# Kernel optimization log

Hardware: AMD Instinct MI355X
Metric: run time of the kernel (lower is better)

Reference implementation:

```python
import jax, jax.numpy as jnp
import numpy as np

# dims: B=8, T=12, N=512, F_in=64, H=8, F'=out_features//H=8
NEG_SLOPE = 0.01  # torch LeakyReLU default


def setup_inputs() -> dict:
    key = jax.random.key(0)
    ks = jax.random.split(key, 8)
    B, T, N, Fin, H, Fp = 8, 12, 512, 64, 8, 8
    x = jax.random.normal(ks[0], (B, T, N, Fin), dtype=jnp.float32)
    # sparse-ish adjacency with guaranteed self loops (avoids all -inf rows)
    adj = (jax.random.uniform(ks[1], (N, N)) < 0.05).astype(jnp.float32)
    adj = jnp.clip(adj + jnp.eye(N, dtype=jnp.float32), 0.0, 1.0)
    # per-head Linear(in_features, F'): stacked weights [H, Fin, F'] + bias [H, F']
    W = jax.random.normal(ks[2], (H, Fin, Fp), dtype=jnp.float32) * 0.1
    Wb = jax.random.normal(ks[3], (H, Fp), dtype=jnp.float32) * 0.1
    # per-head Linear(2F', 1): split into src-half a1 (multiplies h_j, first F'
    # of the concat) and dst-half a2 (multiplies h_i), plus scalar bias ab
    a1 = jax.random.normal(ks[4], (H, Fp), dtype=jnp.float32) * 0.1
    a2 = jax.random.normal(ks[5], (H, Fp), dtype=jnp.float32) * 0.1
    ab = jax.random.normal(ks[6], (H,), dtype=jnp.float32) * 0.1
    return {"x": x, "adj": adj, "W": W, "Wb": Wb, "a1": a1, "a2": a2, "ab": ab}


def reference(x, adj, W, Wb, a1, a2, ab):
    # h[b,t,h,n,f'] = x @ W_h + b_h
    h = jnp.einsum('btni,hio->bthno', x, W) + Wb[:, None, :]
    # a(cat(h_j, h_i)) = a1.h_j + a2.h_i + ab  (exact decomposition of the
    # original broadcast-concat; avoids the O(N^2 * 2F') a_input tensor)
    s_src = jnp.einsum('bthno,ho->bthn', h, a1)  # contributes along j axis
    s_dst = jnp.einsum('bthno,ho->bthn', h, a2)  # contributes along i axis
    e = jax.nn.leaky_relu(
        s_src[..., None, :] + s_dst[..., :, None] + ab[:, None, None],
        negative_slope=NEG_SLOPE,
    )  # [B,T,H,N,N]
    e = jnp.where(adj == 0, -jnp.inf, e)
    attn = jax.nn.softmax(e, axis=-1)  # (dropout is identity in eval mode)
    h_prime = jnp.einsum('bthij,bthjo->bthio', attn, h)  # [B,T,H,N,F']
    B, T, H, N, Fp = h_prime.shape
    # concat heads along feature dim, matching torch.cat(head_outputs, -1)
    return h_prime.transpose(0, 1, 3, 2, 4).reshape(B, T, N, H * Fp)
```

## Files before the change

### kernel.cpp

```cpp
#include <hip/hip_runtime.h>
#include <math.h>

namespace {

constexpr int kN    = 512;
constexpr int kFin  = 64;
constexpr int kH    = 8;
constexpr int kFp   = 8;
constexpr int kBT   = 96;
constexpr int kNT   = 256;
constexpr int kMaxDeg = 104;
constexpr float kNeg = 0.01f;
constexpr float kL2E = 1.44269504088896340736f;

typedef _Float16 half8t __attribute__((ext_vector_type(8)));
typedef unsigned int uint;

__device__ __forceinline__ float fast_exp2(float v) {
#if __has_builtin(__builtin_amdgcn_exp2f)
  return __builtin_amdgcn_exp2f(v);
#else
  return exp2f(v);
#endif
}

constexpr int kOffBits = 0;
constexpr int kOffPerm = kOffBits + kN * 16;
constexpr int kOffDeg  = kOffPerm + kN;
constexpr int kOffRPos = kOffDeg + kN;
constexpr int kOffIdx  = kOffRPos + kN;

__global__ void pack_adj_kernel(const float* __restrict__ adj,
                                uint* __restrict__ bitsR) {
  const int t = blockIdx.x * blockDim.x + threadIdx.x;
  const unsigned long long m = __ballot(adj[t] != 0.0f);
  const int lane = threadIdx.x & 63;
  if ((lane & 31) == 0) {
    const int i = t >> 9;
    const int w = (t & 511) >> 5;
    bitsR[i * 16 + w] = (uint)(m >> (lane & 32));
  }
}

__global__ __launch_bounds__(512) void sort_assign_kernel(
    const uint* __restrict__ bitsR, uint* __restrict__ permG,
    uint* __restrict__ degG, uint* __restrict__ rowpos) {
  __shared__ int base[128];
  const int i = threadIdx.x;
  int deg = 0;
#pragma unroll
  for (int w = 0; w < 16; ++w) deg += __popc(bitsR[i * 16 + w]);
  const int dc = min(deg, 127);

  if (i < 128) base[i] = 0;
  __syncthreads();
  atomicAdd(&base[dc], 1);
  __syncthreads();
  if (i == 0) {
    int run = 0;
    for (int k = 0; k < 128; ++k) {
      const int c = base[k];
      base[k] = run;
      run += c;
    }
  }
  __syncthreads();
  const int pos = atomicAdd(&base[dc], 1);
  permG[pos] = (uint)i;
  degG[pos] = (uint)deg;
  rowpos[i] = (uint)pos;
}

__global__ __launch_bounds__(64) void csr_fill_kernel(
    const uint* __restrict__ bitsR, const uint* __restrict__ rowpos,
    uint* __restrict__ idxG) {
  const int i = blockIdx.x;
  const int l = threadIdx.x;
  const int pos = (int)rowpos[i];
  uint b = (l < 16) ? bitsR[i * 16 + l] : 0u;
  const int cnt = __popc(b);
  int scan = cnt;
#pragma unroll
  for (int off = 1; off < 16; off <<= 1) {
    const int v = __shfl_up(scan, off, 64);
    if (l >= off) scan += v;
  }
  int slot = scan - cnt;
  while (b) {
    const int j = l * 32 + __builtin_ctz(b);
    b &= b - 1;
    idxG[slot * kN + pos] = (uint)j;
    ++slot;
  }
}

__global__ __launch_bounds__(kNT) void gat_sparse_kernel(
    const float* __restrict__ x, const uint* __restrict__ permG,
    const uint* __restrict__ degG, const uint* __restrict__ idxG,
    const float* __restrict__ W, const float* __restrict__ Wb,
    const float* __restrict__ a1, const float* __restrict__ a2,
    const float* __restrict__ ab, float* __restrict__ out) {
  __shared__ _Float16 h16S[kN * 8];
  __shared__ float ssrcS[kN];
  __shared__ float sdstS[kN];

  const int bt  = blockIdx.x % kBT;
  const int h   = blockIdx.x / kBT;
  const int tid = threadIdx.x;

  const float* xb = x + (size_t)bt * kN * kFin;
  const float* Wl = W + h * kFin * kFp;

  float xr0[kFin], xr1[kFin];
  {
    const float4* p0 = reinterpret_cast<const float4*>(xb + (size_t)tid * kFin);
    const float4* p1 =
        reinterpret_cast<const float4*>(xb + (size_t)(tid + kNT) * kFin);
#pragma unroll
    for (int c4 = 0; c4 < kFin / 4; ++c4) {
      *reinterpret_cast<float4*>(&xr0[c4 * 4]) = p0[c4];
      *reinterpret_cast<float4*>(&xr1[c4 * 4]) = p1[c4];
    }
  }

  float acc0[kFp], acc1[kFp];
#pragma unroll
  for (int f = 0; f < kFp; ++f) {
    const float b = Wb[h * kFp + f];
    acc0[f] = b;
    acc1[f] = b;
  }
#pragma unroll
  for (int i = 0; i < kFin; ++i) {
#pragma unroll
    for (int f = 0; f < kFp; ++f) {
      const float wv = Wl[i * kFp + f];
      acc0[f] = fmaf(xr0[i], wv, acc0[f]);
      acc1[f] = fmaf(xr1[i], wv, acc1[f]);
    }
  }

  float s1a = 0.f, s2a = 0.f, s1b = 0.f, s2b = 0.f;
#pragma unroll
  for (int f = 0; f < kFp; ++f) {
    const float A1 = a1[h * kFp + f];
    const float A2 = a2[h * kFp + f];
    s1a = fmaf(acc0[f], A1, s1a);
    s2a = fmaf(acc0[f], A2, s2a);
    s1b = fmaf(acc1[f], A1, s1b);
    s2b = fmaf(acc1[f], A2, s2b);
  }
  const float abh = ab[h];
  ssrcS[tid]       = s1a * kL2E;
  ssrcS[tid + kNT] = s1b * kL2E;
  sdstS[tid]       = (s2a + abh) * kL2E;
  sdstS[tid + kNT] = (s2b + abh) * kL2E;

  {
    half8t hv;
#pragma unroll
    for (int f = 0; f < kFp; ++f) hv[f] = (_Float16)acc0[f];
    *reinterpret_cast<half8t*>(&h16S[(size_t)tid * 8]) = hv;
#pragma unroll
    for (int f = 0; f < kFp; ++f) hv[f] = (_Float16)acc1[f];
    *reinterpret_cast<half8t*>(&h16S[(size_t)(tid + kNT) * 8]) = hv;
  }
  __syncthreads();

  const int p0 = 2 * tid;
  const uint2 ip = *reinterpret_cast<const uint2*>(&permG[p0]);
  const uint2 dp = *reinterpret_cast<const uint2*>(&degG[p0]);
  const int i0 = (int)ip.x, i1 = (int)ip.y;
  const int d0 = (int)dp.x, d1 = (int)dp.y;
  const float sd0 = sdstS[i0];
  const float sd1 = sdstS[i1];
  const int dmax = max(d0, d1);

  float o0[kFp], o1[kFp];
#pragma unroll
  for (int f = 0; f < kFp; ++f) {
    o0[f] = 0.f;
    o1[f] = 0.f;
  }
  float sum0 = 0.f, sum1 = 0.f;

  uint2 jj = *reinterpret_cast<const uint2*>(&idxG[p0]);
#pragma unroll 1
  for (int slot = 0; slot < dmax; ++slot) {
    const uint2 jn =
        *reinterpret_cast<const uint2*>(&idxG[(slot + 1) * kN + p0]);
    const int j0 = (int)(jj.x & 511u);
    const int j1 = (int)(jj.y & 511u);

    const half8t hv0 = *reinterpret_cast<const half8t*>(&h16S[(size_t)j0 * 8]);
    const half8t hv1 = *reinterpret_cast<const half8t*>(&h16S[(size_t)j1 * 8]);
    float e0 = ssrcS[j0] + sd0;
    float e1 = ssrcS[j1] + sd1;
    e0 = fmaxf(e0, e0 * kNeg);
    e1 = fmaxf(e1, e1 * kNeg);
    float q0 = fast_exp2(e0);
    float q1 = fast_exp2(e1);
    q0 = (slot < d0) ? q0 : 0.f;
    q1 = (slot < d1) ? q1 : 0.f;
    sum0 += q0;
    sum1 += q1;
#pragma unroll
    for (int f = 0; f < kFp; ++f) {
      o0[f] = fmaf((float)hv0[f], q0, o0[f]);
      o1[f] = fmaf((float)hv1[f], q1, o1[f]);
    }
    jj = jn;
  }

  const float r0 = 1.0f / sum0;
  const float r1 = 1.0f / sum1;
  float* q0p = out + (((size_t)bt * kN + i0) * kH + h) * kFp;
  float* q1p = out + (((size_t)bt * kN + i1) * kH + h) * kFp;
  reinterpret_cast<float4*>(q0p)[0] =
      make_float4(o0[0] * r0, o0[1] * r0, o0[2] * r0, o0[3] * r0);
  reinterpret_cast<float4*>(q0p)[1] =
      make_float4(o0[4] * r0, o0[5] * r0, o0[6] * r0, o0[7] * r0);
  reinterpret_cast<float4*>(q1p)[0] =
      make_float4(o1[0] * r1, o1[1] * r1, o1[2] * r1, o1[3] * r1);
  reinterpret_cast<float4*>(q1p)[1] =
      make_float4(o1[4] * r1, o1[5] * r1, o1[6] * r1, o1[7] * r1);
}

}

extern "C" void kernel_launch(void* const* d_in, const int* in_sizes, int n_in,
                              void* d_out, int out_size, void* d_ws, size_t ws_size,
                              hipStream_t stream) {
  const float* x   = (const float*)d_in[0];
  const float* adj = (const float*)d_in[1];
  const float* W   = (const float*)d_in[2];
  const float* Wb  = (const float*)d_in[3];
  const float* a1  = (const float*)d_in[4];
  const float* a2  = (const float*)d_in[5];
  const float* ab  = (const float*)d_in[6];
  float* out = (float*)d_out;

  uint* ws     = (uint*)d_ws;
  uint* bitsR  = ws + kOffBits;
  uint* permG  = ws + kOffPerm;
  uint* degG   = ws + kOffDeg;
  uint* rowpos = ws + kOffRPos;
  uint* idxG   = ws + kOffIdx;

  hipLaunchKernelGGL(pack_adj_kernel, dim3(kN * kN / kNT), dim3(kNT), 0, stream,
                     adj, bitsR);
  hipLaunchKernelGGL(sort_assign_kernel, dim3(1), dim3(512), 0, stream,
                     bitsR, permG, degG, rowpos);
  hipLaunchKernelGGL(csr_fill_kernel, dim3(kN), dim3(64), 0, stream,
                     bitsR, rowpos, idxG);
  hipLaunchKernelGGL(gat_sparse_kernel, dim3(kBT * kH), dim3(kNT), 0, stream,
                     x, permG, degG, idxG, W, Wb, a1, a2, ab, out);
}
```

Measured before the change: 107.7 us.

## Fuse degree sort and CSR fill into one rank-based kernel

```diff
diff --git a/kernel.cpp b/kernel.cpp
--- a/kernel.cpp
+++ b/kernel.cpp
@@ -27,8 +27,7 @@
 constexpr int kOffBits = 0;
 constexpr int kOffPerm = kOffBits + kN * 16;
 constexpr int kOffDeg  = kOffPerm + kN;
-constexpr int kOffRPos = kOffDeg + kN;
-constexpr int kOffIdx  = kOffRPos + kN;
+constexpr int kOffIdx  = kOffDeg + kN;
 
 __global__ void pack_adj_kernel(const float* __restrict__ adj,
                                 uint* __restrict__ bitsR) {
@@ -42,50 +41,50 @@
   }
 }
 
-__global__ __launch_bounds__(512) void sort_assign_kernel(
+__global__ __launch_bounds__(64) void rank_fill_kernel(
     const uint* __restrict__ bitsR, uint* __restrict__ permG,
-    uint* __restrict__ degG, uint* __restrict__ rowpos) {
-  __shared__ int base[128];
-  const int i = threadIdx.x;
-  int deg = 0;
-#pragma unroll
-  for (int w = 0; w < 16; ++w) deg += __popc(bitsR[i * 16 + w]);
-  const int dc = min(deg, 127);
-
-  if (i < 128) base[i] = 0;
-  __syncthreads();
-  atomicAdd(&base[dc], 1);
-  __syncthreads();
-  if (i == 0) {
-    int run = 0;
-    for (int k = 0; k < 128; ++k) {
-      const int c = base[k];
-      base[k] = run;
-      run += c;
-    }
-  }
-  __syncthreads();
-  const int pos = atomicAdd(&base[dc], 1);
-  permG[pos] = (uint)i;
-  degG[pos] = (uint)deg;
-  rowpos[i] = (uint)pos;
-}
-
-__global__ __launch_bounds__(64) void csr_fill_kernel(
-    const uint* __restrict__ bitsR, const uint* __restrict__ rowpos,
-    uint* __restrict__ idxG) {
+    uint* __restrict__ degG, uint* __restrict__ idxG) {
+  __shared__ int degS[kN];
   const int i = blockIdx.x;
   const int l = threadIdx.x;
-  const int pos = (int)rowpos[i];
+
+#pragma unroll
+  for (int r8 = 0; r8 < 8; ++r8) {
+    const int r = l + r8 * 64;
+    const uint4* p = reinterpret_cast<const uint4*>(&bitsR[r * 16]);
+    const uint4 a = p[0], b = p[1], c = p[2], d = p[3];
+    degS[r] = __popc(a.x) + __popc(a.y) + __popc(a.z) + __popc(a.w) +
+              __popc(b.x) + __popc(b.y) + __popc(b.z) + __popc(b.w) +
+              __popc(c.x) + __popc(c.y) + __popc(c.z) + __popc(c.w) +
+              __popc(d.x) + __popc(d.y) + __popc(d.z) + __popc(d.w);
+  }
+  __syncthreads();
+
+  const int degi = degS[i];
+  int cnt = 0;
+#pragma unroll
+  for (int r8 = 0; r8 < 8; ++r8) {
+    const int r = l + r8 * 64;
+    const int dr = degS[r];
+    cnt += (dr < degi || (dr == degi && r < i)) ? 1 : 0;
+  }
+#pragma unroll
+  for (int off = 32; off > 0; off >>= 1) cnt += __shfl_xor(cnt, off, 64);
+  const int pos = cnt;
+  if (l == 0) {
+    permG[pos] = (uint)i;
+    degG[pos] = (uint)degi;
+  }
+
   uint b = (l < 16) ? bitsR[i * 16 + l] : 0u;
-  const int cnt = __popc(b);
-  int scan = cnt;
+  const int cntw = __popc(b);
+  int scan = cntw;
 #pragma unroll
   for (int off = 1; off < 16; off <<= 1) {
     const int v = __shfl_up(scan, off, 64);
     if (l >= off) scan += v;
   }
-  int slot = scan - cnt;
+  int slot = scan - cntw;
   while (b) {
     const int j = l * 32 + __builtin_ctz(b);
     b &= b - 1;
@@ -108,18 +107,23 @@
   const int h   = blockIdx.x / kBT;
   const int tid = threadIdx.x;
 
+  const int p0 = 2 * tid;
+  const uint2 ip = *reinterpret_cast<const uint2*>(&permG[p0]);
+  const uint2 dp = *reinterpret_cast<const uint2*>(&degG[p0]);
+  uint2 jj = *reinterpret_cast<const uint2*>(&idxG[p0]);
+
   const float* xb = x + (size_t)bt * kN * kFin;
   const float* Wl = W + h * kFin * kFp;
 
   float xr0[kFin], xr1[kFin];
   {
-    const float4* p0 = reinterpret_cast<const float4*>(xb + (size_t)tid * kFin);
-    const float4* p1 =
+    const float4* px0 = reinterpret_cast<const float4*>(xb + (size_t)tid * kFin);
+    const float4* px1 =
         reinterpret_cast<const float4*>(xb + (size_t)(tid + kNT) * kFin);
 #pragma unroll
     for (int c4 = 0; c4 < kFin / 4; ++c4) {
-      *reinterpret_cast<float4*>(&xr0[c4 * 4]) = p0[c4];
-      *reinterpret_cast<float4*>(&xr1[c4 * 4]) = p1[c4];
+      *reinterpret_cast<float4*>(&xr0[c4 * 4]) = px0[c4];
+      *reinterpret_cast<float4*>(&xr1[c4 * 4]) = px1[c4];
     }
   }
 
@@ -167,9 +171,6 @@
   }
   __syncthreads();
 
-  const int p0 = 2 * tid;
-  const uint2 ip = *reinterpret_cast<const uint2*>(&permG[p0]);
-  const uint2 dp = *reinterpret_cast<const uint2*>(&degG[p0]);
   const int i0 = (int)ip.x, i1 = (int)ip.y;
   const int d0 = (int)dp.x, d1 = (int)dp.y;
   const float sd0 = sdstS[i0];
@@ -184,7 +185,6 @@
   }
   float sum0 = 0.f, sum1 = 0.f;
 
-  uint2 jj = *reinterpret_cast<const uint2*>(&idxG[p0]);
 #pragma unroll 1
   for (int slot = 0; slot < dmax; ++slot) {
     const uint2 jn =
@@ -240,19 +240,16 @@
   const float* ab  = (const float*)d_in[6];
   float* out = (float*)d_out;
 
-  uint* ws     = (uint*)d_ws;
-  uint* bitsR  = ws + kOffBits;
-  uint* permG  = ws + kOffPerm;
-  uint* degG   = ws + kOffDeg;
-  uint* rowpos = ws + kOffRPos;
-  uint* idxG   = ws + kOffIdx;
+  uint* ws    = (uint*)d_ws;
+  uint* bitsR = ws + kOffBits;
+  uint* permG = ws + kOffPerm;
+  uint* degG  = ws + kOffDeg;
+  uint* idxG  = ws + kOffIdx;
 
   hipLaunchKernelGGL(pack_adj_kernel, dim3(kN * kN / kNT), dim3(kNT), 0, stream,
                      adj, bitsR);
-  hipLaunchKernelGGL(sort_assign_kernel, dim3(1), dim3(512), 0, stream,
-                     bitsR, permG, degG, rowpos);
-  hipLaunchKernelGGL(csr_fill_kernel, dim3(kN), dim3(64), 0, stream,
-                     bitsR, rowpos, idxG);
+  hipLaunchKernelGGL(rank_fill_kernel, dim3(kN), dim3(64), 0, stream,
+                     bitsR, permG, degG, idxG);
   hipLaunchKernelGGL(gat_sparse_kernel, dim3(kBT * kH), dim3(kNT), 0, stream,
                      x, permG, degG, idxG, W, Wb, a1, a2, ab, out);
 }
```

Result: faster. 103.5 us (-4.0%).
